# Kernel optimization log

Hardware: AMD Instinct MI355X
Metric: run time of the kernel (lower is better)

The kernel has to match this reference:

```python
import jax, jax.numpy as jnp
import numpy as np
from jax import lax

N, IN, OUT, R, K = 16384, 128, 128, 3, 16
H = IN  # DGL lstm aggregator: LSTM(in_feats, in_feats)


def setup_inputs() -> dict:
    key = jax.random.key(0)
    ks = jax.random.split(key, 10)
    s_in = np.float32(1.0 / np.sqrt(IN))
    return {
        "x": jax.random.normal(ks[0], (N, IN), jnp.float32),
        "conn": jax.random.normal(ks[1], (N, IN), jnp.float32),
        "nbr_idx": jax.random.randint(ks[2], (R, N, K), 0, N),
        "trans": jax.random.normal(ks[3], (OUT, IN), jnp.float32) * s_in,
        "W_ih": jax.random.normal(ks[4], (R, 4 * H, IN), jnp.float32) * s_in,
        "W_hh": jax.random.normal(ks[5], (R, 4 * H, H), jnp.float32) * s_in,
        "b_lstm": jnp.zeros((R, 4 * H), jnp.float32),
        "fc_self": jax.random.normal(ks[6], (R, OUT, IN), jnp.float32) * s_in,
        "fc_neigh": jax.random.normal(ks[7], (R, OUT, H), jnp.float32) * s_in,
        "bias": jnp.zeros((R, OUT), jnp.float32),
    }


def _lstm_last_hidden(seq, Wih, Whh, b):
    """seq: [N, K, IN] neighbor sequence -> final hidden state [N, H].
    PyTorch/DGL gate order: input, forget, cell, output."""
    n = seq.shape[0]
    h0 = jnp.zeros((n, H), seq.dtype)
    c0 = jnp.zeros((n, H), seq.dtype)

    def step(carry, x_t):
        h, c = carry
        gates = x_t @ Wih.T + h @ Whh.T + b  # [N, 4H]
        i, f, g, o = jnp.split(gates, 4, axis=-1)
        i = jax.nn.sigmoid(i)
        f = jax.nn.sigmoid(f)
        o = jax.nn.sigmoid(o)
        g = jnp.tanh(g)
        c = f * c + i * g
        h = o * jnp.tanh(c)
        return (h, c), None

    (h, _), _ = lax.scan(step, (h0, c0), jnp.swapaxes(seq, 0, 1))  # scan over K
    return h


def reference(x, conn, nbr_idx, trans, W_ih, W_hh, b_lstm, fc_self, fc_neigh, bias):
    outs = []
    for r in range(R):  # small fixed relation set
        nbr = x[nbr_idx[r]]  # [N, K, IN] irregular gather
        h_n = _lstm_last_hidden(nbr, W_ih[r], W_hh[r], b_lstm[r])
        o = x @ fc_self[r].T + h_n @ fc_neigh[r].T + bias[r]
        outs.append(jax.nn.leaky_relu(o))  # slope 0.01 == F.leaky_relu default
    X = jnp.stack(outs, axis=1)  # [N, R, OUT]
    # att_score = (X @ trans) @ conn[:, :, None], softmax over relations
    score = jnp.einsum('nrd,di,ni->nr', X, trans, conn)
    att = jax.nn.softmax(score, axis=1)
    return jnp.einsum('nrd,nr->nd', X, att)  # [N, OUT]
```

## Files before the change

### kernel.cpp

```cpp
#include <hip/hip_runtime.h>

#define NN    16384
#define HD    128
#define G4    512
#define KST   16
#define NRELS 3
#define NPB   16
#define LOG2E 1.44269504f
#define TT    2.8853901f

using f16x8 = __attribute__((ext_vector_type(8))) _Float16;
using f32x4 = __attribute__((ext_vector_type(4))) float;

static __device__ __forceinline__ f32x4 f4splat(float v) {
    f32x4 r; r[0] = v; r[1] = v; r[2] = v; r[3] = v; return r;
}
static __device__ __forceinline__ f16x8 load8h(const float* p) {
    const float4 a = ((const float4*)p)[0];
    const float4 b = ((const float4*)p)[1];
    f16x8 r;
    r[0] = (_Float16)a.x; r[1] = (_Float16)a.y; r[2] = (_Float16)a.z; r[3] = (_Float16)a.w;
    r[4] = (_Float16)b.x; r[5] = (_Float16)b.y; r[6] = (_Float16)b.z; r[7] = (_Float16)b.w;
    return r;
}
static __device__ __forceinline__ f16x8 load8hs(const float* p, float s) {
    const float4 a = ((const float4*)p)[0];
    const float4 b = ((const float4*)p)[1];
    f16x8 r;
    r[0] = (_Float16)(a.x * s); r[1] = (_Float16)(a.y * s);
    r[2] = (_Float16)(a.z * s); r[3] = (_Float16)(a.w * s);
    r[4] = (_Float16)(b.x * s); r[5] = (_Float16)(b.y * s);
    r[6] = (_Float16)(b.z * s); r[7] = (_Float16)(b.w * s);
    return r;
}
static __device__ __forceinline__ f32x4 mfma16h(f16x8 a, f16x8 b, f32x4 c) {
    return __builtin_amdgcn_mfma_f32_16x16x32_f16(a, b, c, 0, 0, 0);
}
static __device__ __forceinline__ unsigned short f2h_bits(float f) {
    return __builtin_bit_cast(unsigned short, (_Float16)f);
}
static __device__ __forceinline__ float h2f(unsigned short b) {
    return (float)__builtin_bit_cast(_Float16, b);
}
static __device__ __forceinline__ void barrier_lgkm() {
    asm volatile("s_waitcnt lgkmcnt(0)" ::: "memory");
    __builtin_amdgcn_s_barrier();
}

template <int OUTC, int MODE>
__global__ __launch_bounds__(512, 2) void gemm_rt(
    const float* __restrict__ A, const float* __restrict__ W,
    const float* __restrict__ bias, void* __restrict__ outp)
{
    constexpr int CW = OUTC / 8;
    constexpr int CT = CW / 16;
    const int tid = threadIdx.x;
    const int w = tid >> 6, lane = tid & 63;
    const int g = lane >> 4, m = lane & 15;
    const int n0 = blockIdx.x * 64;
    const int r = blockIdx.y;
    const float* Wr = W + (size_t)r * OUTC * HD;

    f32x4 acc[4][CT];
#pragma unroll
    for (int rt = 0; rt < 4; ++rt)
#pragma unroll
        for (int ct = 0; ct < CT; ++ct) acc[rt][ct] = f4splat(0.0f);

#pragma unroll
    for (int kc = 0; kc < 4; ++kc) {
        f16x8 a[4];
#pragma unroll
        for (int rt = 0; rt < 4; ++rt)
            a[rt] = load8h(A + (size_t)(n0 + rt * 16 + m) * HD + kc * 32 + 8 * g);
        f16x8 b[CT];
#pragma unroll
        for (int ct = 0; ct < CT; ++ct)
            b[ct] = load8h(Wr + (size_t)(w * CW + ct * 16 + m) * HD + kc * 32 + 8 * g);
#pragma unroll
        for (int rt = 0; rt < 4; ++rt)
#pragma unroll
            for (int ct = 0; ct < CT; ++ct)
                acc[rt][ct] = mfma16h(a[rt], b[ct], acc[rt][ct]);
    }

#pragma unroll
    for (int rt = 0; rt < 4; ++rt)
#pragma unroll
        for (int ct = 0; ct < CT; ++ct) {
            const int col = w * CW + ct * 16 + m;
            const float bv = bias ? bias[r * OUTC + col] : 0.0f;
#pragma unroll
            for (int e = 0; e < 4; ++e) {
                const int row = n0 + rt * 16 + 4 * g + e;
                const float v = acc[rt][ct][e] + bv;
                if constexpr (MODE == 0) {
                    ((float*)outp)[(size_t)row * OUTC + col] = v;
                } else {
                    const int q = col >> 7;
                    const float s = (q == 2) ? 2.0f * LOG2E : LOG2E;
                    ((unsigned short*)outp)[((size_t)r * NN + row) * G4 + (size_t)(col & 127) * 4 + q] =
                        f2h_bits(v * s);
                }
            }
        }
}

__global__ __launch_bounds__(512, 4) void lstm_kernel(
    const float* __restrict__ x, const int* __restrict__ nbr,
    const float* __restrict__ Whh, const float* __restrict__ fcs,
    const float* __restrict__ fcn, const float* __restrict__ bias,
    const unsigned short* __restrict__ xW, float* __restrict__ Xout)
{
    __shared__ unsigned short h_lds[2][NPB * HD];
    __shared__ unsigned short xbuf[2][NPB * G4];
    __shared__ int idx_lds[KST * NPB];

    const int tid = threadIdx.x;
    const int w = tid >> 6, lane = tid & 63;
    const int g = lane >> 4, m = lane & 15;
    const int n0 = blockIdx.x * NPB;
    const int r = blockIdx.y;
    const char* xwr = (const char*)(xW + (size_t)r * NN * G4);

    if ((blockIdx.x >> 8) & 1) {
        asm volatile("s_sleep 32");
        asm volatile("s_sleep 22");
    }

    if (tid < KST * NPB) {
        const int t = tid >> 4, n = tid & 15;
        idx_lds[tid] = nbr[((size_t)r * NN + n0 + n) * KST + t] << 10;
    }

    f16x8 bw[4][4];
    const float* whr = Whh + (size_t)r * G4 * HD;
#pragma unroll
    for (int q = 0; q < 4; ++q) {
        const float s = (q == 2) ? 2.0f * LOG2E : LOG2E;
#pragma unroll
        for (int kc = 0; kc < 4; ++kc)
            bw[q][kc] = load8hs(whr + (size_t)(q * 128 + w * 16 + m) * HD + kc * 32 + 8 * g, s);
    }

    int rd_off[4], wr_off[4];
#pragma unroll
    for (int kc = 0; kc < 4; ++kc)
        rd_off[kc] = m * HD + ((kc * 32 + 8 * g) ^ ((m & 7) << 3));
#pragma unroll
    for (int e = 0; e < 4; ++e) {
        const int row = 4 * g + e;
        wr_off[e] = row * HD + ((w * 16 + m) ^ ((row & 7) << 3));
    }
    const int xb_wrA = (2 * w) * G4 + lane * 8;
    const int xb_wrB = (2 * w + 1) * G4 + lane * 8;
    const int xb_rd  = (4 * g) * G4 + (w * 16 + m) * 4;

    float cst[4] = {0.0f, 0.0f, 0.0f, 0.0f};
    __syncthreads();

    uint4 pa, pb;
    {
        const unsigned oa = (unsigned)idx_lds[0 * 16 + 2 * w];
        const unsigned ob = (unsigned)idx_lds[0 * 16 + 2 * w + 1];
        pa = *(const uint4*)(xwr + oa + lane * 16);
        pb = *(const uint4*)(xwr + ob + lane * 16);
        *(uint4*)&xbuf[0][xb_wrA] = pa;
        *(uint4*)&xbuf[0][xb_wrB] = pb;
        const unsigned oa1 = (unsigned)idx_lds[1 * 16 + 2 * w];
        const unsigned ob1 = (unsigned)idx_lds[1 * 16 + 2 * w + 1];
        pa = *(const uint4*)(xwr + oa1 + lane * 16);
        pb = *(const uint4*)(xwr + ob1 + lane * 16);
    }
    barrier_lgkm();

    for (int t = 0; t < KST; ++t) {
        const int rb = t & 1;
        const int wb = rb ^ 1;

        ushort4 xv[4];
#pragma unroll
        for (int e = 0; e < 4; ++e)
            xv[e] = *(const ushort4*)&xbuf[rb][xb_rd + e * G4];

        f32x4 acc[4];
#pragma unroll
        for (int e = 0; e < 4; ++e) {
            acc[0][e] = h2f(xv[e].x);
            acc[1][e] = h2f(xv[e].y);
            acc[2][e] = h2f(xv[e].z);
            acc[3][e] = h2f(xv[e].w);
        }

        __builtin_amdgcn_s_setprio(1);
        if (t > 0) {
            const unsigned short* hb = h_lds[rb];
#pragma unroll
            for (int kc = 0; kc < 4; ++kc) {
                const f16x8 a = *(const f16x8*)&hb[rd_off[kc]];
#pragma unroll
                for (int q = 0; q < 4; ++q)
                    acc[q] = mfma16h(a, bw[q][kc], acc[q]);
            }
        }
        __builtin_amdgcn_s_setprio(0);

        if (t + 1 < KST) {
            *(uint4*)&xbuf[wb][xb_wrA] = pa;
            *(uint4*)&xbuf[wb][xb_wrB] = pb;
            if (t + 2 < KST) {
                const unsigned oa = (unsigned)idx_lds[(t + 2) * 16 + 2 * w];
                const unsigned ob = (unsigned)idx_lds[(t + 2) * 16 + 2 * w + 1];
                pa = *(const uint4*)(xwr + oa + lane * 16);
                pb = *(const uint4*)(xwr + ob + lane * 16);
            }
        }

        unsigned short* nh = h_lds[wb];
#pragma unroll
        for (int e = 0; e < 4; ++e) {
            const float Ai = __builtin_amdgcn_exp2f(-acc[0][e]);
            const float Af = __builtin_amdgcn_exp2f(-acc[1][e]);
            const float Ag = __builtin_amdgcn_exp2f(-acc[2][e]);
            const float Ao = __builtin_amdgcn_exp2f(-acc[3][e]);
            const float Di = 1.0f + Ai, Df = 1.0f + Af;
            const float Dg = 1.0f + Ag, Do = 1.0f + Ao;
            const float DiDg = Di * Dg;
            const float P  = __builtin_fmaf(-TT, Ag, TT);
            const float num = __builtin_fmaf(cst[e], DiDg, P * Df);
            const float R1 = __builtin_amdgcn_rcpf(Df * DiDg);
            const float csn = num * R1;
            cst[e] = csn;
            const float C2 = __builtin_amdgcn_exp2f(-csn);
            const float R2 = __builtin_amdgcn_rcpf(Do * (1.0f + C2));
            nh[wr_off[e]] = f2h_bits((1.0f - C2) * R2);
        }
        barrier_lgkm();
    }

    {
        const unsigned short* hb = h_lds[0];
        const float* fsr = fcs + (size_t)r * HD * HD;
        const float* fnr = fcn + (size_t)r * HD * HD;
        const int col = w * 16 + m;
        f32x4 oacc = f4splat(bias[r * HD + col]);
#pragma unroll
        for (int kc = 0; kc < 4; ++kc) {
            const f16x8 ax = load8h(x + (size_t)(n0 + m) * HD + kc * 32 + 8 * g);
            const f16x8 ah = *(const f16x8*)&hb[rd_off[kc]];
            const f16x8 bs = load8h(fsr + (size_t)col * HD + kc * 32 + 8 * g);
            const f16x8 bn = load8h(fnr + (size_t)col * HD + kc * 32 + 8 * g);
            oacc = mfma16h(ax, bs, oacc);
            oacc = mfma16h(ah, bn, oacc);
        }
#pragma unroll
        for (int e = 0; e < 4; ++e) {
            const int row = 4 * g + e;
            float v = oacc[e];
            v = v > 0.0f ? v : 0.01f * v;
            Xout[((size_t)(n0 + row) * NRELS + r) * HD + col] = v;
        }
    }
}

__global__ __launch_bounds__(256) void attn_kernel(
    const float* __restrict__ X, const float* __restrict__ tc,
    float* __restrict__ out)
{
    const int wv = blockIdx.x * (blockDim.x >> 6) + (threadIdx.x >> 6);
    const int lane = threadIdx.x & 63;
    if (wv >= NN) return;
    const size_t nb = (size_t)wv;

    const float t0 = tc[nb * HD + lane];
    const float t1 = tc[nb * HD + 64 + lane];
    float x0[3], x1[3], sc[3];
#pragma unroll
    for (int r = 0; r < 3; ++r) {
        x0[r] = X[(nb * 3 + r) * HD + lane];
        x1[r] = X[(nb * 3 + r) * HD + 64 + lane];
        float p = x0[r] * t0 + x1[r] * t1;
#pragma unroll
        for (int off = 32; off >= 1; off >>= 1)
            p += __shfl_xor(p, off, 64);
        sc[r] = p;
    }
    const float mx = fmaxf(sc[0], fmaxf(sc[1], sc[2]));
    const float e0 = __expf(sc[0] - mx), e1 = __expf(sc[1] - mx), e2 = __expf(sc[2] - mx);
    const float inv = __builtin_amdgcn_rcpf(e0 + e1 + e2);
    const float a0 = e0 * inv, a1 = e1 * inv, a2 = e2 * inv;
    out[nb * HD + lane]      = a0 * x0[0] + a1 * x0[1] + a2 * x0[2];
    out[nb * HD + 64 + lane] = a0 * x1[0] + a1 * x1[1] + a2 * x1[2];
}

extern "C" void kernel_launch(void* const* d_in, const int* in_sizes, int n_in,
                              void* d_out, int out_size, void* d_ws, size_t ws_size,
                              hipStream_t stream)
{
    const float* x     = (const float*)d_in[0];
    const float* conn  = (const float*)d_in[1];
    const int*   nbr   = (const int*)d_in[2];
    const float* trans = (const float*)d_in[3];
    const float* Wih   = (const float*)d_in[4];
    const float* Whh   = (const float*)d_in[5];
    const float* blstm = (const float*)d_in[6];
    const float* fcs   = (const float*)d_in[7];
    const float* fcn   = (const float*)d_in[8];
    const float* bias  = (const float*)d_in[9];
    float* out = (float*)d_out;

    const size_t XW_B = (size_t)NRELS * NN * G4 * 2;
    const size_t TC_B = (size_t)NN * HD * 4;
    const size_t XO_B = (size_t)NN * NRELS * HD * 4;
    if (ws_size < XW_B + TC_B + XO_B) return;

    char* wsb = (char*)d_ws;
    unsigned short* xW = (unsigned short*)wsb;
    float*          tc = (float*)(wsb + XW_B);
    float*          Xo = (float*)(wsb + XW_B + TC_B);

    gemm_rt<512, 1><<<dim3(NN / 64, NRELS), 512, 0, stream>>>(x, Wih, blstm, (void*)xW);
    gemm_rt<128, 0><<<dim3(NN / 64, 1), 512, 0, stream>>>(conn, trans, nullptr, (void*)tc);
    lstm_kernel<<<dim3(NN / NPB, NRELS), 512, 0, stream>>>(x, nbr, Whh, fcs, fcn, bias, xW, Xo);
    attn_kernel<<<dim3(NN / 4), 256, 0, stream>>>(Xo, tc, out);
}
```

Before: 313.5 us.

## Replace LSTM step barriers with per-wave LDS flags and direct gathered loads

The per-timestep workgroup barrier is replaced by per-wave progress flags in LDS. Each wave spin-waits only on the two waves that produced the h-chunk it needs, and walks the chunks in a staggered order. The gathered xW rows are no longer staged through an LDS double buffer; each lane loads its ushort4 gate inputs straight from global memory one step ahead. The s_sleep staggering and setprio hints are dropped. This removes barrier stalls and LDS traffic, at the cost of spin-polling overhead and narrower, less coalesced global loads.

```diff
diff --git a/kernel.cpp b/kernel.cpp
--- a/kernel.cpp
+++ b/kernel.cpp
@@ -41,10 +41,6 @@
 }
 static __device__ __forceinline__ float h2f(unsigned short b) {
     return (float)__builtin_bit_cast(_Float16, b);
-}
-static __device__ __forceinline__ void barrier_lgkm() {
-    asm volatile("s_waitcnt lgkmcnt(0)" ::: "memory");
-    __builtin_amdgcn_s_barrier();
 }
 
 template <int OUTC, int MODE>
@@ -113,25 +109,22 @@
     const unsigned short* __restrict__ xW, float* __restrict__ Xout)
 {
     __shared__ unsigned short h_lds[2][NPB * HD];
-    __shared__ unsigned short xbuf[2][NPB * G4];
     __shared__ int idx_lds[KST * NPB];
+    __shared__ int flags[8];
 
     const int tid = threadIdx.x;
     const int w = tid >> 6, lane = tid & 63;
     const int g = lane >> 4, m = lane & 15;
     const int n0 = blockIdx.x * NPB;
     const int r = blockIdx.y;
+    const unsigned laneoff = (unsigned)(w * 16 + m) * 8u;
     const char* xwr = (const char*)(xW + (size_t)r * NN * G4);
-
-    if ((blockIdx.x >> 8) & 1) {
-        asm volatile("s_sleep 32");
-        asm volatile("s_sleep 22");
-    }
 
     if (tid < KST * NPB) {
         const int t = tid >> 4, n = tid & 15;
         idx_lds[tid] = nbr[((size_t)r * NN + n0 + n) * KST + t] << 10;
     }
+    if (tid < 8) flags[tid] = 0;
 
     f16x8 bw[4][4];
     const float* whr = Whh + (size_t)r * G4 * HD;
@@ -152,36 +145,23 @@
         const int row = 4 * g + e;
         wr_off[e] = row * HD + ((w * 16 + m) ^ ((row & 7) << 3));
     }
-    const int xb_wrA = (2 * w) * G4 + lane * 8;
-    const int xb_wrB = (2 * w + 1) * G4 + lane * 8;
-    const int xb_rd  = (4 * g) * G4 + (w * 16 + m) * 4;
 
     float cst[4] = {0.0f, 0.0f, 0.0f, 0.0f};
     __syncthreads();
 
-    uint4 pa, pb;
+    ushort4 xv[4];
     {
-        const unsigned oa = (unsigned)idx_lds[0 * 16 + 2 * w];
-        const unsigned ob = (unsigned)idx_lds[0 * 16 + 2 * w + 1];
-        pa = *(const uint4*)(xwr + oa + lane * 16);
-        pb = *(const uint4*)(xwr + ob + lane * 16);
-        *(uint4*)&xbuf[0][xb_wrA] = pa;
-        *(uint4*)&xbuf[0][xb_wrB] = pb;
-        const unsigned oa1 = (unsigned)idx_lds[1 * 16 + 2 * w];
-        const unsigned ob1 = (unsigned)idx_lds[1 * 16 + 2 * w + 1];
-        pa = *(const uint4*)(xwr + oa1 + lane * 16);
-        pb = *(const uint4*)(xwr + ob1 + lane * 16);
-    }
-    barrier_lgkm();
-
+        const int4 i4 = *(const int4*)&idx_lds[4 * g];
+        xv[0] = *(const ushort4*)(xwr + (unsigned)i4.x + laneoff);
+        xv[1] = *(const ushort4*)(xwr + (unsigned)i4.y + laneoff);
+        xv[2] = *(const ushort4*)(xwr + (unsigned)i4.z + laneoff);
+        xv[3] = *(const ushort4*)(xwr + (unsigned)i4.w + laneoff);
+    }
+
+    const volatile int* vfl = (const volatile int*)flags;
     for (int t = 0; t < KST; ++t) {
         const int rb = t & 1;
         const int wb = rb ^ 1;
-
-        ushort4 xv[4];
-#pragma unroll
-        for (int e = 0; e < 4; ++e)
-            xv[e] = *(const ushort4*)&xbuf[rb][xb_rd + e * G4];
 
         f32x4 acc[4];
 #pragma unroll
@@ -192,27 +172,26 @@
             acc[3][e] = h2f(xv[e].w);
         }
 
-        __builtin_amdgcn_s_setprio(1);
+        if (t + 1 < KST) {
+            const int4 i4 = *(const int4*)&idx_lds[(t + 1) * 16 + 4 * g];
+            xv[0] = *(const ushort4*)(xwr + (unsigned)i4.x + laneoff);
+            xv[1] = *(const ushort4*)(xwr + (unsigned)i4.y + laneoff);
+            xv[2] = *(const ushort4*)(xwr + (unsigned)i4.z + laneoff);
+            xv[3] = *(const ushort4*)(xwr + (unsigned)i4.w + laneoff);
+        }
+
         if (t > 0) {
             const unsigned short* hb = h_lds[rb];
 #pragma unroll
-            for (int kc = 0; kc < 4; ++kc) {
+            for (int kk = 0; kk < 4; ++kk) {
+                const int kc = ((w >> 1) + kk) & 3;
+                const int p0 = 2 * kc;
+                while (vfl[p0] < t || vfl[p0 + 1] < t) {}
+                __builtin_amdgcn_sched_barrier(0);
                 const f16x8 a = *(const f16x8*)&hb[rd_off[kc]];
 #pragma unroll
                 for (int q = 0; q < 4; ++q)
                     acc[q] = mfma16h(a, bw[q][kc], acc[q]);
-            }
-        }
-        __builtin_amdgcn_s_setprio(0);
-
-        if (t + 1 < KST) {
-            *(uint4*)&xbuf[wb][xb_wrA] = pa;
-            *(uint4*)&xbuf[wb][xb_wrB] = pb;
-            if (t + 2 < KST) {
-                const unsigned oa = (unsigned)idx_lds[(t + 2) * 16 + 2 * w];
-                const unsigned ob = (unsigned)idx_lds[(t + 2) * 16 + 2 * w + 1];
-                pa = *(const uint4*)(xwr + oa + lane * 16);
-                pb = *(const uint4*)(xwr + ob + lane * 16);
             }
         }
 
@@ -235,9 +214,14 @@
             const float R2 = __builtin_amdgcn_rcpf(Do * (1.0f + C2));
             nh[wr_off[e]] = f2h_bits((1.0f - C2) * R2);
         }
-        barrier_lgkm();
-    }
-
+        asm volatile("s_waitcnt lgkmcnt(0)" ::: "memory");
+        if (lane == 0) ((volatile int*)flags)[w] = t + 1;
+    }
+
+#pragma unroll
+    for (int p = 0; p < 8; ++p)
+        while (vfl[p] < KST) {}
+    __builtin_amdgcn_sched_barrier(0);
     {
         const unsigned short* hb = h_lds[0];
         const float* fsr = fcs + (size_t)r * HD * HD;
```

After: 1.181 ms. 3.77x slower.
